# Performance work log

Measured on AMD Instinct MI355X. Metric: run time of the kernel, lower is better.

## Reference

```python
import jax, jax.numpy as jnp
import numpy as np

SCALE = 0.02
EPS = 1e-5


def setup_inputs() -> dict:
    key = jax.random.key(0)
    ks = jax.random.split(key, 11)
    C = 256
    inp = {
        "x": jax.random.normal(ks[0], (64, C, 28, 28), dtype=jnp.float32),
        "w1": jax.random.normal(ks[1], (C, C, 3, 3), dtype=jnp.float32) * 0.05,
        "g1": jax.random.uniform(ks[2], (C,), dtype=jnp.float32, minval=0.5, maxval=1.5),
        "b1": jax.random.normal(ks[3], (C,), dtype=jnp.float32) * 0.1,
        "m1": jax.random.normal(ks[4], (C,), dtype=jnp.float32) * 0.1,
        "v1": jax.random.uniform(ks[5], (C,), dtype=jnp.float32, minval=0.5, maxval=1.5),
        "w2": jax.random.normal(ks[6], (C, C, 3, 3), dtype=jnp.float32) * 0.05,
        "g2": jax.random.uniform(ks[7], (C,), dtype=jnp.float32, minval=0.5, maxval=1.5),
        "b2": jax.random.normal(ks[8], (C,), dtype=jnp.float32) * 0.1,
        "m2": jax.random.normal(ks[9], (C,), dtype=jnp.float32) * 0.1,
        "v2": jax.random.uniform(ks[10], (C,), dtype=jnp.float32, minval=0.5, maxval=1.5),
    }
    return inp


def _bin_conv3x3(x, w, stride=1):
    # 1-bit weight conv: sign(w)*scale, straight-through estimator for grads.
    wb = w + jax.lax.stop_gradient(jnp.sign(w) - w)
    y = jax.lax.conv_general_dilated(
        x, wb,
        window_strides=(stride, stride),
        padding=[(1, 1), (1, 1)],
        dimension_numbers=("NCHW", "OIHW", "NCHW"),
    )
    return y * SCALE


def _bn(x, g, b, m, v):
    # eval-mode batchnorm with running stats
    inv = g * jax.lax.rsqrt(v + EPS)  # [C]
    return x * inv[None, :, None, None] + (b - m * inv)[None, :, None, None]


def reference(x, w1, g1, b1, m1, v1, w2, g2, b2, m2, v2):
    out = jax.nn.relu(_bn(_bin_conv3x3(x, w1, 1), g1, b1, m1, v1))
    out = _bn(_bin_conv3x3(out, w2, 1), g2, b2, m2, v2)
    return jax.nn.relu(out + x)
```

## Files before the change

kernel.cpp:

```cpp
#include <hip/hip_runtime.h>

#define EPS_F 1e-5f
#define SCALE_F 0.02f

using short8  = __attribute__((ext_vector_type(8))) short;
using floatx4 = __attribute__((ext_vector_type(4))) float;

__device__ __forceinline__ unsigned short f2bf(float f) {
  unsigned u = __float_as_uint(f);
  return (unsigned short)((u + 0x7fffu + ((u >> 16) & 1u)) >> 16);
}

__global__ void prep_w(const float* __restrict__ w1, const float* __restrict__ w2,
                       unsigned short* __restrict__ ap1, unsigned short* __restrict__ ap2,
                       const float* g1, const float* b1, const float* m1, const float* v1,
                       const float* g2, const float* b2, const float* m2, const float* v2,
                       float* bnp) {
  const float* __restrict__ w = blockIdx.y ? w2 : w1;
  unsigned short* __restrict__ ap = blockIdx.y ? ap2 : ap1;
  int t = blockIdx.x * 256 + threadIdx.x;
  int off = t >> 13;
  int c8  = (t >> 8) & 31;
  int co  = t & 255;
  const float* ws = w + (size_t)(co * 256 + c8 * 8) * 9 + off;
  short8 o;
#pragma unroll
  for (int j = 0; j < 8; ++j) {
    float v = ws[j * 9];
    o[j] = (v > 0.f) ? (short)0x3F80 : ((v < 0.f) ? (short)0xBF80 : (short)0);
  }
  *(short8*)(ap + (size_t)t * 8) = o;
  if (blockIdx.x == 0 && blockIdx.y == 0) {
    int c = threadIdx.x;
    float i1 = g1[c] * rsqrtf(v1[c] + EPS_F);
    bnp[c]       = SCALE_F * i1;
    bnp[256 + c] = b1[c] - m1[c] * i1;
    float i2 = g2[c] * rsqrtf(v2[c] + EPS_F);
    bnp[512 + c] = SCALE_F * i2;
    bnp[768 + c] = b2[c] - m2[c] * i2;
  }
}

__global__ void prep_x(const float* __restrict__ x, unsigned short* __restrict__ xb,
                       unsigned short* __restrict__ abuf) {
  int h = blockIdx.x;
  int n = blockIdx.y;
  int tid = threadIdx.x;
  const float* xs = x + ((size_t)n * 256 + tid) * 784 + h * 28;
  unsigned short* xd = xb + ((size_t)n * 900 + (h + 1) * 30 + 1) * 256 + tid;
#pragma unroll
  for (int p4 = 0; p4 < 7; ++p4) {
    floatx4 f = *(const floatx4*)(xs + p4 * 4);
#pragma unroll
    for (int k = 0; k < 4; ++k)
      xd[(size_t)(p4 * 4 + k) * 256] = f2bf(f[k]);
  }
  {
    int bufi = tid >> 7, side = (tid >> 6) & 1, c4 = tid & 63;
    unsigned short* bb = (bufi ? abuf : xb) + ((size_t)n * 900 + (h + 1) * 30 + side * 29) * 256;
    ushort4 z = {0, 0, 0, 0};
    *(ushort4*)(bb + c4 * 4) = z;
  }
  if (h == 0 || h == 27) {
    int row = (h == 0) ? 0 : 29;
    for (int u = tid; u < 3840; u += 256) {
      int bufi = u / 1920;
      int r    = u - bufi * 1920;
      int px   = r >> 6, c4 = r & 63;
      unsigned short* bb = (bufi ? abuf : xb) + ((size_t)n * 900 + row * 30 + px) * 256;
      ushort4 z = {0, 0, 0, 0};
      *(ushort4*)(bb + c4 * 4) = z;
    }
  }
}

template<int STAGE>
__global__ __launch_bounds__(256, 2) void bconv(
    const unsigned short* __restrict__ Bin,
    const unsigned short* __restrict__ Apack,
    const float* __restrict__ bnp,
    unsigned short* __restrict__ aout,
    const float* __restrict__ xres,
    float* __restrict__ out)
{
  __shared__ __align__(16) unsigned short smem[STAGE == 1 ? 29568 : 11520];
  unsigned short* Blds = smem;

  const int tid  = threadIdx.x;
  const int lane = tid & 63;
  const int wv   = tid >> 6;
  const int quad = lane >> 4;
  const int l16  = lane & 15;
  const int spBlk = blockIdx.x;
  const int n     = blockIdx.y;

  const int prow0 = 4 * spBlk;
  const unsigned short* bsrc = Bin + ((size_t)n * 900 + prow0 * 30) * 256;
  const int coW = wv * 64;

  int pxS[7];
#pragma unroll
  for (int s = 0; s < 7; ++s) {
    int lm = s * 16 + l16;
    int hl = lm / 28;
    int w  = lm - hl * 28;
    pxS[s] = hl * 30 + w;
  }

  floatx4 acc[4][7];
#pragma unroll
  for (int c = 0; c < 4; ++c)
#pragma unroll
    for (int s = 0; s < 7; ++s)
      acc[c][s] = (floatx4){0.f, 0.f, 0.f, 0.f};

#pragma unroll 1
  for (int cb = 0; cb < 4; ++cb) {
    __syncthreads();
    for (int u = tid; u < 1440; u += 256) {
      int px = u >> 3, c = u & 7;
      const unsigned short* src = bsrc + (size_t)px * 256 + cb * 64 + c * 8;
      *(short8*)&Blds[(px << 6) + ((c ^ (px & 7)) << 3)] = *(const short8*)src;
    }
    __syncthreads();

    const int cq = cb * 8 + quad;
#pragma unroll 1
    for (int kh = 0; kh < 3; ++kh) {
#pragma unroll
      for (int kw = 0; kw < 3; ++kw) {
        const int D = kh * 30 + kw;
        const int chunk0 = (kh * 3 + kw) * 32 + cq;
#pragma unroll
        for (int half = 0; half < 2; ++half) {
          const int chunk = chunk0 + half * 4;
          const unsigned short* apb = Apack + ((size_t)(chunk * 256 + coW + l16)) * 8;
          short8 a0 = *(const short8*)(apb);
          short8 a1 = *(const short8*)(apb + 16 * 8);
          short8 a2 = *(const short8*)(apb + 32 * 8);
          short8 a3 = *(const short8*)(apb + 48 * 8);
          const int C = half * 4 + quad;
#pragma unroll
          for (int s = 0; s < 7; ++s) {
            int pe = pxS[s] + D;
            short8 b = *(const short8*)&Blds[(pe << 6) + ((C ^ (pe & 7)) << 3)];
            acc[0][s] = __builtin_amdgcn_mfma_f32_16x16x32_bf16(a0, b, acc[0][s], 0, 0, 0);
            acc[1][s] = __builtin_amdgcn_mfma_f32_16x16x32_bf16(a1, b, acc[1][s], 0, 0, 0);
            acc[2][s] = __builtin_amdgcn_mfma_f32_16x16x32_bf16(a2, b, acc[2][s], 0, 0, 0);
            acc[3][s] = __builtin_amdgcn_mfma_f32_16x16x32_bf16(a3, b, acc[3][s], 0, 0, 0);
          }
        }
      }
    }
  }

  if (STAGE == 1) {
    __syncthreads();
#pragma unroll
    for (int c = 0; c < 4; ++c) {
      int co = coW + c * 16 + quad * 4;
      floatx4 As = *(const floatx4*)(bnp + co);
      floatx4 Bs = *(const floatx4*)(bnp + 256 + co);
#pragma unroll
      for (int s = 0; s < 7; ++s) {
        int px = s * 16 + l16;
        ushort4 o;
        o.x = f2bf(fmaxf(acc[c][s][0] * As[0] + Bs[0], 0.f));
        o.y = f2bf(fmaxf(acc[c][s][1] * As[1] + Bs[1], 0.f));
        o.z = f2bf(fmaxf(acc[c][s][2] * As[2] + Bs[2], 0.f));
        o.w = f2bf(fmaxf(acc[c][s][3] * As[3] + Bs[3], 0.f));
        *(ushort4*)&smem[px * 264 + co] = o;
      }
    }
    __syncthreads();
    unsigned short* dst0 = aout + ((size_t)n * 900 + (prow0 + 1) * 30 + 1) * 256;
    for (int u = tid; u < 3584; u += 256) {
      int px = u >> 5;
      int c8 = (u & 31) * 8;
      int r  = px / 28;
      int w  = px - r * 28;
      *(short8*)(dst0 + (size_t)(r * 30 + w) * 256 + c8) = *(const short8*)&smem[px * 264 + c8];
    }
  } else {
#pragma unroll
    for (int c = 0; c < 4; ++c) {
      int co = coW + c * 16 + quad * 4;
      floatx4 As = *(const floatx4*)(bnp + 512 + co);
      floatx4 Bs = *(const floatx4*)(bnp + 768 + co);
#pragma unroll
      for (int s = 0; s < 7; ++s) {
        int m = spBlk * 112 + s * 16 + l16;
#pragma unroll
        for (int r = 0; r < 4; ++r) {
          size_t oidx = ((size_t)n * 256 + co + r) * 784 + m;
          float v = acc[c][s][r] * As[r] + Bs[r] + xres[oidx];
          out[oidx] = fmaxf(v, 0.f);
        }
      }
    }
  }
}


extern "C" void kernel_launch(void* const* d_in, const int* in_sizes, int n_in,
                              void* d_out, int out_size, void* d_ws, size_t ws_size,
                              hipStream_t stream) {
  const float* x  = (const float*)d_in[0];
  const float* w1 = (const float*)d_in[1];
  const float* g1 = (const float*)d_in[2];
  const float* b1 = (const float*)d_in[3];
  const float* m1 = (const float*)d_in[4];
  const float* v1 = (const float*)d_in[5];
  const float* w2 = (const float*)d_in[6];
  const float* g2 = (const float*)d_in[7];
  const float* b2 = (const float*)d_in[8];
  const float* m2 = (const float*)d_in[9];
  const float* v2 = (const float*)d_in[10];
  float* out = (float*)d_out;

  char* ws = (char*)d_ws;
  const size_t PADBUF = (size_t)64 * 900 * 256 * 2;
  const size_t WPACK  = 589824ull * 2;
  unsigned short* xb   = (unsigned short*)ws;
  unsigned short* abuf = (unsigned short*)(ws + PADBUF);
  unsigned short* ap1  = (unsigned short*)(ws + 2 * PADBUF);
  unsigned short* ap2  = (unsigned short*)(ws + 2 * PADBUF + WPACK);
  float* bnp           = (float*)(ws + 2 * PADBUF + 2 * WPACK);

  prep_w<<<dim3(288, 2), 256, 0, stream>>>(w1, w2, ap1, ap2,
                                           g1, b1, m1, v1, g2, b2, m2, v2, bnp);
  prep_x<<<dim3(28, 64), 256, 0, stream>>>(x, xb, abuf);

  dim3 grid(7, 64);
  bconv<1><<<grid, 256, 0, stream>>>(xb,   ap1, bnp, abuf, nullptr, nullptr);
  bconv<2><<<grid, 256, 0, stream>>>(abuf, ap2, bnp, nullptr, x, out);
}
```

Measured before the change: 249.8 us.

## Double-buffer LDS input tiles with register-staged prefetch and raise MFMA priority

Replaces the load-sync-compute loop over channel blocks with an LDS double buffer. The next channel block's global data is prefetched into registers at the start of each iteration and written to the alternate LDS buffer after compute, which removes one barrier per iteration and hides global latency behind the MFMA work. It also wraps the MFMA bursts in s_setprio to favour this wave's matrix issue. The cost is 48 extra VGPRs for staging, which could cause spills under the 2-blocks-per-SM launch bound, and stage 2 now uses twice the LDS.

```diff
diff --git a/kernel.cpp b/kernel.cpp
--- a/kernel.cpp
+++ b/kernel.cpp
@@ -74,6 +74,37 @@
   }
 }
 
+__device__ __forceinline__ void stage_load(const unsigned short* __restrict__ bsrc,
+                                           int cb, int tid, short8* stg) {
+  const unsigned short* __restrict__ b = bsrc + cb * 64;
+#pragma unroll
+  for (int i = 0; i < 5; ++i) {
+    int u = tid + i * 256;
+    int px = u >> 3, c = u & 7;
+    stg[i] = *(const short8*)(b + (size_t)px * 256 + c * 8);
+  }
+  if (tid < 160) {
+    int u = tid + 1280;
+    int px = u >> 3, c = u & 7;
+    stg[5] = *(const short8*)(b + (size_t)px * 256 + c * 8);
+  }
+}
+
+__device__ __forceinline__ void stage_write(unsigned short* __restrict__ B,
+                                            int tid, const short8* stg) {
+#pragma unroll
+  for (int i = 0; i < 5; ++i) {
+    int u = tid + i * 256;
+    int px = u >> 3, c = u & 7;
+    *(short8*)&B[(px << 6) + ((c ^ (px & 7)) << 3)] = stg[i];
+  }
+  if (tid < 160) {
+    int u = tid + 1280;
+    int px = u >> 3, c = u & 7;
+    *(short8*)&B[(px << 6) + ((c ^ (px & 7)) << 3)] = stg[5];
+  }
+}
+
 template<int STAGE>
 __global__ __launch_bounds__(256, 2) void bconv(
     const unsigned short* __restrict__ Bin,
@@ -83,8 +114,7 @@
     const float* __restrict__ xres,
     float* __restrict__ out)
 {
-  __shared__ __align__(16) unsigned short smem[STAGE == 1 ? 29568 : 11520];
-  unsigned short* Blds = smem;
+  __shared__ __align__(16) unsigned short smem[STAGE == 1 ? 29568 : 23040];
 
   const int tid  = threadIdx.x;
   const int lane = tid & 63;
@@ -114,15 +144,17 @@
     for (int s = 0; s < 7; ++s)
       acc[c][s] = (floatx4){0.f, 0.f, 0.f, 0.f};
 
+  short8 stg[6];
+
+  stage_load(bsrc, 0, tid, stg);
+  stage_write(smem, tid, stg);
+  __syncthreads();
+
 #pragma unroll 1
   for (int cb = 0; cb < 4; ++cb) {
-    __syncthreads();
-    for (int u = tid; u < 1440; u += 256) {
-      int px = u >> 3, c = u & 7;
-      const unsigned short* src = bsrc + (size_t)px * 256 + cb * 64 + c * 8;
-      *(short8*)&Blds[(px << 6) + ((c ^ (px & 7)) << 3)] = *(const short8*)src;
-    }
-    __syncthreads();
+    unsigned short* Blds = smem + (cb & 1) * 11520;
+
+    if (cb < 3) stage_load(bsrc, cb + 1, tid, stg);
 
     const int cq = cb * 8 + quad;
 #pragma unroll 1
@@ -140,6 +172,7 @@
           short8 a2 = *(const short8*)(apb + 32 * 8);
           short8 a3 = *(const short8*)(apb + 48 * 8);
           const int C = half * 4 + quad;
+          __builtin_amdgcn_s_setprio(1);
 #pragma unroll
           for (int s = 0; s < 7; ++s) {
             int pe = pxS[s] + D;
@@ -149,8 +182,14 @@
             acc[2][s] = __builtin_amdgcn_mfma_f32_16x16x32_bf16(a2, b, acc[2][s], 0, 0, 0);
             acc[3][s] = __builtin_amdgcn_mfma_f32_16x16x32_bf16(a3, b, acc[3][s], 0, 0, 0);
           }
+          __builtin_amdgcn_s_setprio(0);
         }
       }
+    }
+
+    if (cb < 3) {
+      stage_write(smem + ((cb + 1) & 1) * 11520, tid, stg);
+      __syncthreads();
     }
   }
 
```

After: 243.4 us. 2.5% less time.

## Double-buffer LDS with async global_load_lds and prefetch weights in conv loop

Applied to the files above, without the earlier changes.

Replaces the synchronous per-channel-block LDS staging with double-buffered asynchronous global-to-LDS loads, so the next block's activations are fetched while MFMAs run on the current buffer. Weight fragments are software-pipelined one tap ahead in registers, and MFMA sections are wrapped in s_setprio. Block indices are remapped with a swizzle that changes which blocks run concurrently, which may affect L2 locality. This raises register pressure and LDS usage for stage 2, and relies on the wait semantics of the async LDS loads being handled correctly at the barriers.

```diff
diff --git a/kernel.cpp b/kernel.cpp
--- a/kernel.cpp
+++ b/kernel.cpp
@@ -83,16 +83,18 @@
     const float* __restrict__ xres,
     float* __restrict__ out)
 {
-  __shared__ __align__(16) unsigned short smem[STAGE == 1 ? 29568 : 11520];
-  unsigned short* Blds = smem;
+  __shared__ __align__(16) unsigned short smem[STAGE == 1 ? 29568 : 24576];
 
   const int tid  = threadIdx.x;
   const int lane = tid & 63;
   const int wv   = tid >> 6;
   const int quad = lane >> 4;
   const int l16  = lane & 15;
-  const int spBlk = blockIdx.x;
-  const int n     = blockIdx.y;
+
+  int flat = blockIdx.y * 7 + blockIdx.x;
+  int idx  = (flat & 7) * 56 + (flat >> 3);
+  const int n     = idx / 7;
+  const int spBlk = idx - n * 7;
 
   const int prow0 = 4 * spBlk;
   const unsigned short* bsrc = Bin + ((size_t)n * 900 + prow0 * 30) * 256;
@@ -107,6 +109,51 @@
     pxS[s] = hl * 30 + w;
   }
 
+  int goff0, goff1, goff2, goff3, goff4, goff5;
+  {
+#define MKGOFF(dst, r) { int v = (r) * 256 + tid; int px = v >> 3; \
+    if (px > 179) px = 179; int c = (v & 7) ^ (px & 7); dst = px * 256 + c * 8; }
+    MKGOFF(goff0, 0) MKGOFF(goff1, 1) MKGOFF(goff2, 2)
+    MKGOFF(goff3, 3) MKGOFF(goff4, 4) MKGOFF(goff5, 5)
+#undef MKGOFF
+  }
+
+#define STAGE_CB(cbi, bufsel) { \
+  unsigned short* lb = smem + (bufsel) * 12288 + wv * 512; \
+  const unsigned short* gb = bsrc + (cbi) * 64; \
+  __builtin_amdgcn_global_load_lds((const __attribute__((address_space(1))) void*)(gb + goff0), \
+      (__attribute__((address_space(3))) void*)(lb + 0 * 2048), 16, 0, 0); \
+  __builtin_amdgcn_global_load_lds((const __attribute__((address_space(1))) void*)(gb + goff1), \
+      (__attribute__((address_space(3))) void*)(lb + 1 * 2048), 16, 0, 0); \
+  __builtin_amdgcn_global_load_lds((const __attribute__((address_space(1))) void*)(gb + goff2), \
+      (__attribute__((address_space(3))) void*)(lb + 2 * 2048), 16, 0, 0); \
+  __builtin_amdgcn_global_load_lds((const __attribute__((address_space(1))) void*)(gb + goff3), \
+      (__attribute__((address_space(3))) void*)(lb + 3 * 2048), 16, 0, 0); \
+  __builtin_amdgcn_global_load_lds((const __attribute__((address_space(1))) void*)(gb + goff4), \
+      (__attribute__((address_space(3))) void*)(lb + 4 * 2048), 16, 0, 0); \
+  __builtin_amdgcn_global_load_lds((const __attribute__((address_space(1))) void*)(gb + goff5), \
+      (__attribute__((address_space(3))) void*)(lb + 5 * 2048), 16, 0, 0); }
+
+#define LOADA(d0, d1, d2, d3, t, half, CQ8) { \
+  const unsigned short* p = Apack + ((size_t)(((t) * 32 + (CQ8) + (half) * 4) * 256 + coW + l16)) * 8; \
+  d0 = *(const short8*)p; \
+  d1 = *(const short8*)(p + 128); \
+  d2 = *(const short8*)(p + 256); \
+  d3 = *(const short8*)(p + 384); }
+
+#define HALFMMA(a0, a1, a2, a3, Cx, Dv) { \
+  __builtin_amdgcn_s_setprio(1); \
+  _Pragma("unroll") \
+  for (int s = 0; s < 7; ++s) { \
+    int pe = pxS[s] + (Dv); \
+    short8 b = *(const short8*)&Blds[(pe << 6) + (((Cx) ^ (pe & 7)) << 3)]; \
+    acc[0][s] = __builtin_amdgcn_mfma_f32_16x16x32_bf16(a0, b, acc[0][s], 0, 0, 0); \
+    acc[1][s] = __builtin_amdgcn_mfma_f32_16x16x32_bf16(a1, b, acc[1][s], 0, 0, 0); \
+    acc[2][s] = __builtin_amdgcn_mfma_f32_16x16x32_bf16(a2, b, acc[2][s], 0, 0, 0); \
+    acc[3][s] = __builtin_amdgcn_mfma_f32_16x16x32_bf16(a3, b, acc[3][s], 0, 0, 0); \
+  } \
+  __builtin_amdgcn_s_setprio(0); }
+
   floatx4 acc[4][7];
 #pragma unroll
   for (int c = 0; c < 4; ++c)
@@ -114,43 +161,31 @@
     for (int s = 0; s < 7; ++s)
       acc[c][s] = (floatx4){0.f, 0.f, 0.f, 0.f};
 
+  short8 A0, A1, A2, A3, N0, N1, N2, N3;
+
+  STAGE_CB(0, 0);
+  LOADA(A0, A1, A2, A3, 0, 0, quad);
+  LOADA(N0, N1, N2, N3, 0, 1, quad);
+  __syncthreads();
+
 #pragma unroll 1
   for (int cb = 0; cb < 4; ++cb) {
-    __syncthreads();
-    for (int u = tid; u < 1440; u += 256) {
-      int px = u >> 3, c = u & 7;
-      const unsigned short* src = bsrc + (size_t)px * 256 + cb * 64 + c * 8;
-      *(short8*)&Blds[(px << 6) + ((c ^ (px & 7)) << 3)] = *(const short8*)src;
-    }
-    __syncthreads();
-
-    const int cq = cb * 8 + quad;
+    unsigned short* Blds = smem + (cb & 1) * 12288;
+    if (cb < 3) STAGE_CB(cb + 1, (cb + 1) & 1);
+    const int cq8 = cb * 8 + quad;
+    int D = 0;
 #pragma unroll 1
-    for (int kh = 0; kh < 3; ++kh) {
-#pragma unroll
-      for (int kw = 0; kw < 3; ++kw) {
-        const int D = kh * 30 + kw;
-        const int chunk0 = (kh * 3 + kw) * 32 + cq;
-#pragma unroll
-        for (int half = 0; half < 2; ++half) {
-          const int chunk = chunk0 + half * 4;
-          const unsigned short* apb = Apack + ((size_t)(chunk * 256 + coW + l16)) * 8;
-          short8 a0 = *(const short8*)(apb);
-          short8 a1 = *(const short8*)(apb + 16 * 8);
-          short8 a2 = *(const short8*)(apb + 32 * 8);
-          short8 a3 = *(const short8*)(apb + 48 * 8);
-          const int C = half * 4 + quad;
-#pragma unroll
-          for (int s = 0; s < 7; ++s) {
-            int pe = pxS[s] + D;
-            short8 b = *(const short8*)&Blds[(pe << 6) + ((C ^ (pe & 7)) << 3)];
-            acc[0][s] = __builtin_amdgcn_mfma_f32_16x16x32_bf16(a0, b, acc[0][s], 0, 0, 0);
-            acc[1][s] = __builtin_amdgcn_mfma_f32_16x16x32_bf16(a1, b, acc[1][s], 0, 0, 0);
-            acc[2][s] = __builtin_amdgcn_mfma_f32_16x16x32_bf16(a2, b, acc[2][s], 0, 0, 0);
-            acc[3][s] = __builtin_amdgcn_mfma_f32_16x16x32_bf16(a3, b, acc[3][s], 0, 0, 0);
-          }
-        }
-      }
+    for (int t = 0; t < 9; ++t) {
+      HALFMMA(A0, A1, A2, A3, quad, D);
+      if (t < 8) LOADA(A0, A1, A2, A3, t + 1, 0, cq8);
+      HALFMMA(N0, N1, N2, N3, 4 + quad, D);
+      if (t < 8) LOADA(N0, N1, N2, N3, t + 1, 1, cq8);
+      D += (t == 2 || t == 5) ? 28 : 1;
+    }
+    if (cb < 3) {
+      LOADA(A0, A1, A2, A3, 0, 0, cq8 + 8);
+      LOADA(N0, N1, N2, N3, 0, 1, cq8 + 8);
+      __syncthreads();
     }
   }
 
@@ -199,6 +234,9 @@
       }
     }
   }
+#undef STAGE_CB
+#undef LOADA
+#undef HALFMMA
 }
 
 
```

Result: faster. 230.7 us (-7.6%).
